# Kernel tuning notes

Measured on AMD Instinct MI355X. Metric: run time of the kernel, lower is better.

## Reference

```python
import jax, jax.numpy as jnp
import numpy as np

N_HEADS = 8
EPS = 1e-12  # F.normalize eps


def setup_inputs() -> dict:
    key = jax.random.key(0)
    ks = jax.random.split(key, 7)
    B, M, S, D = 2, 4, 2048, 512
    scale = 1.0 / np.sqrt(D)
    return {
        "x": jax.random.normal(ks[0], (B, M, S, D), dtype=jnp.float32),
        "Wq": jax.random.normal(ks[1], (D, D), dtype=jnp.float32) * scale,
        "bq": jax.random.normal(ks[2], (D,), dtype=jnp.float32) * 0.01,
        "Wkv": jax.random.normal(ks[3], (D, D), dtype=jnp.float32) * scale,
        "bkv": jax.random.normal(ks[4], (D,), dtype=jnp.float32) * 0.01,
        "Wo": jax.random.normal(ks[5], (D, D), dtype=jnp.float32) * scale,
        "bo": jax.random.normal(ks[6], (D,), dtype=jnp.float32) * 0.01,
    }


def _heads(t, H):
    # [B,M,S,D] -> [B,M,H,S,dk]
    B, Mo, S, D = t.shape
    return t.reshape(B, Mo, S, H, D // H).swapaxes(2, 3)


def reference(x, Wq, bq, Wkv, bkv, Wo, bo):
    B, Mo, S, D = x.shape
    H = N_HEADS
    # nn.Linear: y = x @ W^T + b
    Q = x @ Wq.T + bq
    KV = x @ Wkv.T + bkv  # K and V share this projection
    Qh = _heads(Q, H)
    Kh = _heads(KV, H)
    Vh = Kh
    # L2-normalize along head dim (cosine attention)
    Qn = Qh / jnp.maximum(jnp.linalg.norm(Qh, axis=-1, keepdims=True), EPS)
    Kn = Kh / jnp.maximum(jnp.linalg.norm(Kh, axis=-1, keepdims=True), EPS)
    scores = jnp.einsum("bmhqd,bmhkd->bmhqk", Qn, Kn)
    attn = jax.nn.softmax(scores, axis=-1)  # dropout=0 (eval)
    ctx = jnp.einsum("bmhqk,bmhkd->bmhqd", attn, Vh)
    ctx = ctx.swapaxes(2, 3).reshape(B, Mo, S, D)
    return ctx @ Wo.T + bo
```

## Files before the change

kernel.cpp:

```cpp
#include <hip/hip_runtime.h>

typedef __attribute__((ext_vector_type(8))) short bf16x8;
typedef __attribute__((ext_vector_type(8))) _Float16 f16x8;
typedef __attribute__((ext_vector_type(2))) _Float16 f16x2;
typedef __attribute__((ext_vector_type(4))) float f32x4;

__device__ __forceinline__ unsigned short f2bf(float f) {
  union { float f; unsigned int i; } v;
  v.f = f;
  unsigned int r = v.i + 0x7FFFu + ((v.i >> 16) & 1u);
  return (unsigned short)(r >> 16);
}

__device__ __forceinline__ f16x2 cvt_pk(float a, float b) {
  return __builtin_bit_cast(f16x2, __builtin_amdgcn_cvt_pkrtz(a, b));
}

__device__ __forceinline__ void gl_lds16(const unsigned short* g, unsigned short* l) {
  __builtin_amdgcn_global_load_lds(
      (const __attribute__((address_space(1))) unsigned int*)g,
      (__attribute__((address_space(3))) unsigned int*)l, 16, 0, 0);
}

__device__ __forceinline__ f16x2 exp_poly(f16x2 x) {
  const f16x2 a5 = {(_Float16)0.00868682f, (_Float16)0.00868682f};
  const f16x2 a4 = {(_Float16)0.04379392f, (_Float16)0.04379392f};
  const f16x2 a3 = {(_Float16)0.16648887f, (_Float16)0.16648887f};
  const f16x2 a2 = {(_Float16)0.49919676f, (_Float16)0.49919676f};
  const f16x2 a1 = {(_Float16)1.00002229f, (_Float16)1.00002229f};
  const f16x2 a0 = {(_Float16)1.00004478f, (_Float16)1.00004478f};
#if __has_builtin(__builtin_elementwise_fma)
  f16x2 r = a5;
  r = __builtin_elementwise_fma(r, x, a4);
  r = __builtin_elementwise_fma(r, x, a3);
  r = __builtin_elementwise_fma(r, x, a2);
  r = __builtin_elementwise_fma(r, x, a1);
  r = __builtin_elementwise_fma(r, x, a0);
#else
  f16x2 r = a5;
  r = r * x + a4;
  r = r * x + a3;
  r = r * x + a2;
  r = r * x + a1;
  r = r * x + a0;
#endif
  return r;
}

__global__ __launch_bounds__(256) void cvt_all(
    const float* __restrict__ x, const float* __restrict__ wq,
    const float* __restrict__ wkv, const float* __restrict__ wo,
    unsigned short* __restrict__ xf, unsigned short* __restrict__ wqf,
    unsigned short* __restrict__ wkvf, unsigned short* __restrict__ wof) {
  int b = blockIdx.x;
  const float* in;
  unsigned short* out;
  int i;
  if (b < 8192) { in = x; out = xf; i = b * 256 + threadIdx.x; }
  else if (b < 8448) { in = wq; out = wqf; i = (b - 8192) * 256 + threadIdx.x; }
  else if (b < 8704) { in = wkv; out = wkvf; i = (b - 8448) * 256 + threadIdx.x; }
  else { in = wo; out = wof; i = (b - 8704) * 256 + threadIdx.x; }
  float4 v = ((const float4*)in)[i];
  int f = i << 2;
  int row = f >> 9, c = f & 511;
  long off = ((((long)(row >> 7) * 8 + (c >> 6)) * 16 + ((row >> 4) & 7) * 2 +
               ((c >> 5) & 1)) * 64 + ((c >> 3) & 3) * 16 + (row & 15)) * 8 + (c & 7);
  ushort4 o;
  o.x = f2bf(v.x);
  o.y = f2bf(v.y);
  o.z = f2bf(v.z);
  o.w = f2bf(v.w);
  *(ushort4*)(out + off) = o;
}

__global__ __launch_bounds__(256) void gemm_qkv(
    const unsigned short* __restrict__ xf, const unsigned short* __restrict__ Wqf,
    const unsigned short* __restrict__ Wkvf, const float* __restrict__ bq,
    const float* __restrict__ bkv, unsigned short* __restrict__ Qn,
    unsigned short* __restrict__ Kf, unsigned short* __restrict__ Vf) {
  __shared__ __attribute__((aligned(16))) unsigned short lA[16 * 512];
  __shared__ __attribute__((aligned(16))) unsigned short lB[16 * 512];
  const int isKV = (int)(blockIdx.y >> 2);
  const unsigned short* Btf = isKV ? Wkvf : Wqf;
  const float* bias = isKV ? bkv : bq;
  const int tid = threadIdx.x;
  const int lane = tid & 63;
  const int quad = lane >> 4, m16 = lane & 15;
  const int w = tid >> 6;
  const int wm = w >> 1, wn = w & 1;
  const long mb = (long)blockIdx.x * 128;
  const int nt = (int)(blockIdx.y & 3);
  const long nb = (long)nt * 128;
  f32x4 acc[4][4];
#pragma unroll
  for (int i = 0; i < 4; i++)
#pragma unroll
    for (int j = 0; j < 4; j++) acc[i][j] = (f32x4){0.f, 0.f, 0.f, 0.f};

  for (int kb = 0; kb < 8; kb++) {
    __syncthreads();
    {
      const unsigned short* gA =
          xf + (((long)blockIdx.x * 8 + kb) * 16 + 4 * w) * 512 + lane * 8;
      gl_lds16(gA, &lA[(4 * w + 0) * 512]);
      gl_lds16(gA + 512, &lA[(4 * w + 1) * 512]);
      gl_lds16(gA + 1024, &lA[(4 * w + 2) * 512]);
      gl_lds16(gA + 1536, &lA[(4 * w + 3) * 512]);
      const unsigned short* gB =
          Btf + (((long)nt * 8 + kb) * 16 + 4 * w) * 512 + lane * 8;
      gl_lds16(gB, &lB[(4 * w + 0) * 512]);
      gl_lds16(gB + 512, &lB[(4 * w + 1) * 512]);
      gl_lds16(gB + 1024, &lB[(4 * w + 2) * 512]);
      gl_lds16(gB + 1536, &lB[(4 * w + 3) * 512]);
    }
    __syncthreads();
#pragma unroll
    for (int ks = 0; ks < 2; ks++) {
      bf16x8 af[4], bfr[4];
#pragma unroll
      for (int i = 0; i < 4; i++)
        af[i] = *(const bf16x8*)&lA[(((wm * 4 + i) << 1) | ks) * 512 + lane * 8];
#pragma unroll
      for (int j = 0; j < 4; j++)
        bfr[j] = *(const bf16x8*)&lB[(((wn * 4 + j) << 1) | ks) * 512 + lane * 8];
#pragma unroll
      for (int i = 0; i < 4; i++)
#pragma unroll
        for (int j = 0; j < 4; j++)
          acc[i][j] =
              __builtin_amdgcn_mfma_f32_16x16x32_bf16(af[i], bfr[j], acc[i][j], 0, 0, 0);
    }
  }
  const int h = (int)(nb >> 6) + wn;
#pragma unroll
  for (int i = 0; i < 4; i++) {
    long row0 = mb + wm * 64 + i * 16 + quad * 4;
    float bb[4], val[4][4], inv[4];
#pragma unroll
    for (int j = 0; j < 4; j++) {
      bb[j] = bias[nb + wn * 64 + j * 16 + m16];
#pragma unroll
      for (int r = 0; r < 4; r++) val[j][r] = acc[i][j][r] + bb[j];
    }
#pragma unroll
    for (int r = 0; r < 4; r++) {
      float s = val[0][r] * val[0][r] + val[1][r] * val[1][r] +
                val[2][r] * val[2][r] + val[3][r] * val[3][r];
      s += __shfl_xor(s, 1);
      s += __shfl_xor(s, 2);
      s += __shfl_xor(s, 4);
      s += __shfl_xor(s, 8);
      inv[r] = 1.0f / fmaxf(sqrtf(s), 1e-12f);
    }
    if (!isKV) {
#pragma unroll
      for (int r = 0; r < 4; r++)
#pragma unroll
        for (int j = 0; j < 4; j++) {
          long col = nb + wn * 64 + j * 16 + m16;
          Qn[(row0 + r) * 512 + col] = f2bf(val[j][r] * inv[r]);
        }
    } else {
      const int bm = (int)(row0 >> 11);
      const int g = bm * 8 + h;
      const int kt = (int)((row0 & 2047) >> 6);
      const long tb = ((long)g * 32 + kt) * 8;
#pragma unroll
      for (int j = 0; j < 4; j++) {
        long kb0 = (tb + i * 2 + (j >> 1)) * 512 +
                   (((((j & 1) << 1) | (m16 >> 3)) * 16 + quad * 4) * 8) + (m16 & 7);
#pragma unroll
        for (int r = 0; r < 4; r++) Kf[kb0 + r * 8] = f2bf(val[j][r] * inv[r]);
      }
#pragma unroll
      for (int j = 0; j < 4; j++) {
        long vo = (tb + j * 2 + (i >> 1)) * 512 +
                  ((((((i & 1) << 1) | (quad >> 1)) * 16 + m16)) * 8) + (quad & 1) * 4;
        f16x2 lo = cvt_pk(val[j][0], val[j][1]);
        f16x2 hi = cvt_pk(val[j][2], val[j][3]);
        uint2 pk = make_uint2(__builtin_bit_cast(unsigned int, lo),
                              __builtin_bit_cast(unsigned int, hi));
        *(uint2*)(Vf + vo) = pk;
      }
    }
  }
}

__global__ __launch_bounds__(256) void gemm_o(
    const unsigned short* __restrict__ Af, const unsigned short* __restrict__ Btf,
    const float* __restrict__ bias, float* __restrict__ Cout) {
  __shared__ __attribute__((aligned(16))) unsigned short lA[16 * 512];
  __shared__ __attribute__((aligned(16))) unsigned short lB[16 * 512];
  const int tid = threadIdx.x;
  const int lane = tid & 63;
  const int quad = lane >> 4, m16 = lane & 15;
  const int w = tid >> 6;
  const int wm = w >> 1, wn = w & 1;
  const long mb = (long)blockIdx.x * 128;
  const int nt = (int)blockIdx.y;
  const long nb = (long)nt * 128;
  f32x4 acc[4][4];
#pragma unroll
  for (int i = 0; i < 4; i++)
#pragma unroll
    for (int j = 0; j < 4; j++) acc[i][j] = (f32x4){0.f, 0.f, 0.f, 0.f};

  for (int kb = 0; kb < 8; kb++) {
    __syncthreads();
    {
      const unsigned short* gA =
          Af + (((long)blockIdx.x * 8 + kb) * 16 + 4 * w) * 512 + lane * 8;
      gl_lds16(gA, &lA[(4 * w + 0) * 512]);
      gl_lds16(gA + 512, &lA[(4 * w + 1) * 512]);
      gl_lds16(gA + 1024, &lA[(4 * w + 2) * 512]);
      gl_lds16(gA + 1536, &lA[(4 * w + 3) * 512]);
      const unsigned short* gB =
          Btf + (((long)nt * 8 + kb) * 16 + 4 * w) * 512 + lane * 8;
      gl_lds16(gB, &lB[(4 * w + 0) * 512]);
      gl_lds16(gB + 512, &lB[(4 * w + 1) * 512]);
      gl_lds16(gB + 1024, &lB[(4 * w + 2) * 512]);
      gl_lds16(gB + 1536, &lB[(4 * w + 3) * 512]);
    }
    __syncthreads();
#pragma unroll
    for (int ks = 0; ks < 2; ks++) {
      bf16x8 af[4], bfr[4];
#pragma unroll
      for (int i = 0; i < 4; i++)
        af[i] = *(const bf16x8*)&lA[(((wm * 4 + i) << 1) | ks) * 512 + lane * 8];
#pragma unroll
      for (int j = 0; j < 4; j++)
        bfr[j] = *(const bf16x8*)&lB[(((wn * 4 + j) << 1) | ks) * 512 + lane * 8];
#pragma unroll
      for (int i = 0; i < 4; i++)
#pragma unroll
        for (int j = 0; j < 4; j++)
          acc[i][j] =
              __builtin_amdgcn_mfma_f32_16x16x32_bf16(af[i], bfr[j], acc[i][j], 0, 0, 0);
    }
  }
#pragma unroll
  for (int i = 0; i < 4; i++) {
    long row0 = mb + wm * 64 + i * 16 + quad * 4;
#pragma unroll
    for (int j = 0; j < 4; j++) {
      long col = nb + wn * 64 + j * 16 + m16;
      float bb = bias[col];
#pragma unroll
      for (int r = 0; r < 4; r++) Cout[(row0 + r) * 512 + col] = acc[i][j][r] + bb;
    }
  }
}

__global__ __launch_bounds__(512, 4) void attn_cos(
    const unsigned short* __restrict__ Qn, const unsigned short* __restrict__ Kf,
    const unsigned short* __restrict__ Vf, unsigned short* __restrict__ ctxf) {
  __shared__ __attribute__((aligned(16))) unsigned short lK[2][8 * 512];
  __shared__ __attribute__((aligned(16))) unsigned short lVt[2][8 * 512];
  __shared__ __attribute__((aligned(16))) unsigned short lP[256 * 64];
  const int id = (int)blockIdx.x;
  const int g = ((id >> 6) << 3) | (id & 7);
  const int qt = (id >> 3) & 7;
  const int bm = g >> 3, h = g & 7;
  const int tid = threadIdx.x;
  const int lane = tid & 63;
  const int quad = lane >> 4, m16 = lane & 15;
  const int w = tid >> 6;
  const long qrow0 = (long)bm * 2048 + qt * 256 + w * 32;
  const int colbase = h * 64;
  const int swz = (m16 & 7) << 3;
  unsigned short* myP = lP + (w * 32) * 64;

  bf16x8 qf[2][2];
#pragma unroll
  for (int i = 0; i < 2; i++)
#pragma unroll
    for (int ks = 0; ks < 2; ks++)
      qf[i][ks] = *(const bf16x8*)(Qn + (qrow0 + i * 16 + m16) * 512 + colbase +
                                   ks * 32 + quad * 8);

  f32x4 cacc[2][4];
#pragma unroll
  for (int i = 0; i < 2; i++)
#pragma unroll
    for (int j = 0; j < 4; j++) cacc[i][j] = (f32x4){0.f, 0.f, 0.f, 0.f};
  f32x4 cacc_l[2];
  cacc_l[0] = (f32x4){0.f, 0.f, 0.f, 0.f};
  cacc_l[1] = (f32x4){0.f, 0.f, 0.f, 0.f};
  const f16x8 onesv = {(_Float16)1.0f, (_Float16)1.0f, (_Float16)1.0f, (_Float16)1.0f,
                       (_Float16)1.0f, (_Float16)1.0f, (_Float16)1.0f, (_Float16)1.0f};

  {
    const long tb0 = (long)g * 32 * 8;
    gl_lds16(Kf + (tb0 + w) * 512 + lane * 8, &lK[0][w * 512]);
    gl_lds16(Vf + (tb0 + w) * 512 + lane * 8, &lVt[0][w * 512]);
  }
  __syncthreads();

  int cur = 0;
  for (int kt = 0; kt < 32; ++kt) {
    {
      const int ktn = (kt + 1) & 31;
      const long tbn = ((long)g * 32 + ktn) * 8;
      gl_lds16(Kf + (tbn + w) * 512 + lane * 8, &lK[cur ^ 1][w * 512]);
      gl_lds16(Vf + (tbn + w) * 512 + lane * 8, &lVt[cur ^ 1][w * 512]);
    }

    f32x4 sacc[2][4];
#pragma unroll
    for (int i = 0; i < 2; i++)
#pragma unroll
      for (int j = 0; j < 4; j++) sacc[i][j] = (f32x4){0.f, 0.f, 0.f, 0.f};
#pragma unroll
    for (int ks = 0; ks < 2; ++ks) {
      bf16x8 kfr[4];
#pragma unroll
      for (int j = 0; j < 4; j++)
        kfr[j] = *(const bf16x8*)&lK[cur][((j << 1) | ks) * 512 + lane * 8];
#pragma unroll
      for (int j = 0; j < 4; j++)
#pragma unroll
        for (int i = 0; i < 2; i++)
          sacc[i][j] = __builtin_amdgcn_mfma_f32_16x16x32_bf16(kfr[j], qf[i][ks],
                                                               sacc[i][j], 0, 0, 0);
    }

#pragma unroll
    for (int i = 0; i < 2; i++)
#pragma unroll
      for (int j = 0; j < 4; j++) {
        f16x2 x01 = cvt_pk(sacc[i][j][0], sacc[i][j][1]);
        f16x2 x23 = cvt_pk(sacc[i][j][2], sacc[i][j][3]);
        f16x2 e01 = exp_poly(x01);
        f16x2 e23 = exp_poly(x23);
        uint2 pk2 = make_uint2(__builtin_bit_cast(unsigned int, e01),
                               __builtin_bit_cast(unsigned int, e23));
        *(uint2*)&myP[(i * 16 + m16) * 64 + ((j * 16 + quad * 4) ^ swz)] = pk2;
      }

#pragma unroll
    for (int ks = 0; ks < 2; ++ks) {
      f16x8 vfr[4];
#pragma unroll
      for (int j = 0; j < 4; j++)
        vfr[j] = *(const f16x8*)&lVt[cur][((j << 1) | ks) * 512 + lane * 8];
      f16x8 pfr[2];
#pragma unroll
      for (int i = 0; i < 2; i++)
        pfr[i] = *(const f16x8*)&myP[(i * 16 + m16) * 64 +
                                     ((ks * 32 + quad * 8) ^ swz)];
#pragma unroll
      for (int i = 0; i < 2; i++) {
#pragma unroll
        for (int j = 0; j < 4; j++)
          cacc[i][j] = __builtin_amdgcn_mfma_f32_16x16x32_f16(pfr[i], vfr[j],
                                                              cacc[i][j], 0, 0, 0);
        cacc_l[i] =
            __builtin_amdgcn_mfma_f32_16x16x32_f16(pfr[i], onesv, cacc_l[i], 0, 0, 0);
      }
    }

    __syncthreads();
    cur ^= 1;
  }

  float linv[2][4];
#pragma unroll
  for (int i = 0; i < 2; i++)
#pragma unroll
    for (int r = 0; r < 4; r++) linv[i][r] = 1.0f / cacc_l[i][r];
  const long cb0 = (((long)(bm * 16 + qt * 2 + (w >> 2)) * 8 + h) * 16);
#pragma unroll
  for (int i = 0; i < 2; i++)
#pragma unroll
    for (int j = 0; j < 4; j++) {
      long off = (cb0 + ((w & 3) * 2 + i) * 2 + (j >> 1)) * 512 +
                 (((((j & 1) << 1) | (m16 >> 3)) * 16 + quad * 4) * 8) + (m16 & 7);
#pragma unroll
      for (int r = 0; r < 4; r++)
        ctxf[off + r * 8] = f2bf(cacc[i][j][r] * linv[i][r]);
    }
}

extern "C" void kernel_launch(void* const* d_in, const int* in_sizes, int n_in,
                              void* d_out, int out_size, void* d_ws, size_t ws_size,
                              hipStream_t stream) {
  (void)in_sizes; (void)n_in; (void)out_size; (void)ws_size;
  const float* x = (const float*)d_in[0];
  const float* Wq = (const float*)d_in[1];
  const float* bq = (const float*)d_in[2];
  const float* Wkv = (const float*)d_in[3];
  const float* bkv = (const float*)d_in[4];
  const float* Wo = (const float*)d_in[5];
  const float* bo = (const float*)d_in[6];

  char* ws = (char*)d_ws;
  unsigned short* xf     = (unsigned short*)(ws);
  unsigned short* Wqf    = (unsigned short*)(ws + 16777216);
  unsigned short* Wkvf   = (unsigned short*)(ws + 17301504);
  unsigned short* Wof    = (unsigned short*)(ws + 17825792);
  unsigned short* Qn_bf  = (unsigned short*)(ws + 18350080);
  unsigned short* Kf     = (unsigned short*)(ws + 35127296);
  unsigned short* Vf     = (unsigned short*)(ws + 51904512);
  unsigned short* ctxf   = xf;

  cvt_all<<<8960, 256, 0, stream>>>(x, Wq, Wkv, Wo, xf, Wqf, Wkvf, Wof);

  gemm_qkv<<<dim3(128, 8), 256, 0, stream>>>(xf, Wqf, Wkvf, bq, bkv, Qn_bf, Kf, Vf);

  attn_cos<<<512, 512, 0, stream>>>(Qn_bf, Kf, Vf, ctxf);

  gemm_o<<<dim3(128, 4), 256, 0, stream>>>(ctxf, Wof, bo, (float*)d_out);
}
```

Measured before the change: 219.7 us.

## Switch attention to 32x32x16 MFMA and keep P in registers via permlane swap

Result: slower. 229.6 us (+4.5%).

```diff
diff --git a/kernel.cpp b/kernel.cpp
--- a/kernel.cpp
+++ b/kernel.cpp
@@ -4,6 +4,8 @@
 typedef __attribute__((ext_vector_type(8))) _Float16 f16x8;
 typedef __attribute__((ext_vector_type(2))) _Float16 f16x2;
 typedef __attribute__((ext_vector_type(4))) float f32x4;
+typedef __attribute__((ext_vector_type(16))) float f32x16;
+typedef __attribute__((ext_vector_type(2))) unsigned int u32x2;
 
 __device__ __forceinline__ unsigned short f2bf(float f) {
   union { float f; unsigned int i; } v;
@@ -14,6 +16,35 @@
 
 __device__ __forceinline__ f16x2 cvt_pk(float a, float b) {
   return __builtin_bit_cast(f16x2, __builtin_amdgcn_cvt_pkrtz(a, b));
+}
+
+__device__ __forceinline__ unsigned as_u32(f16x2 x) {
+  return __builtin_bit_cast(unsigned int, x);
+}
+__device__ __forceinline__ f16x2 as_f16x2(unsigned x) {
+  return __builtin_bit_cast(f16x2, x);
+}
+
+#if __has_builtin(__builtin_amdgcn_permlane32_swap)
+__device__ __forceinline__ u32x2 plswap(unsigned a, unsigned b) {
+  return __builtin_amdgcn_permlane32_swap(a, b, false, false);
+}
+#else
+__device__ __forceinline__ u32x2 plswap(unsigned a, unsigned b) {
+  unsigned pa = (unsigned)__shfl_xor((int)a, 32);
+  unsigned pb = (unsigned)__shfl_xor((int)b, 32);
+  int hi = (int)(threadIdx.x & 32);
+  u32x2 r;
+  r.x = hi ? pb : a;
+  r.y = hi ? b : pa;
+  return r;
+}
+#endif
+
+__device__ __forceinline__ f16x8 pack4(f16x2 a, f16x2 b, f16x2 c, f16x2 d) {
+  union { f16x2 h[4]; f16x8 v; } u;
+  u.h[0] = a; u.h[1] = b; u.h[2] = c; u.h[3] = d;
+  return u.v;
 }
 
 __device__ __forceinline__ void gl_lds16(const unsigned short* g, unsigned short* l) {
@@ -45,6 +76,15 @@
   r = r * x + a0;
 #endif
   return r;
+}
+
+__device__ __forceinline__ float dot2acc(f16x2 a, float acc) {
+#if __has_builtin(__builtin_amdgcn_fdot2)
+  const f16x2 one2 = {(_Float16)1.0f, (_Float16)1.0f};
+  return __builtin_amdgcn_fdot2(a, one2, acc, false);
+#else
+  return acc + (float)a.x + (float)a.y;
+#endif
 }
 
 __global__ __launch_bounds__(256) void cvt_all(
@@ -161,25 +201,25 @@
           Qn[(row0 + r) * 512 + col] = f2bf(val[j][r] * inv[r]);
         }
     } else {
-      const int bm = (int)(row0 >> 11);
-      const int g = bm * 8 + h;
+      const int bm2 = (int)(row0 >> 11);
+      const int gq = bm2 * 8 + h;
       const int kt = (int)((row0 & 2047) >> 6);
-      const long tb = ((long)g * 32 + kt) * 8;
+      const long tb = ((long)gq * 32 + kt) * 8;
 #pragma unroll
       for (int j = 0; j < 4; j++) {
-        long kb0 = (tb + i * 2 + (j >> 1)) * 512 +
-                   (((((j & 1) << 1) | (m16 >> 3)) * 16 + quad * 4) * 8) + (m16 & 7);
+        long kb0 = (tb + (i >> 1) * 4 + j) * 512 +
+                   ((((i & 1) * 16 + quad * 4) | ((m16 >> 3) << 5)) * 8) + (m16 & 7);
 #pragma unroll
         for (int r = 0; r < 4; r++) Kf[kb0 + r * 8] = f2bf(val[j][r] * inv[r]);
       }
 #pragma unroll
       for (int j = 0; j < 4; j++) {
-        long vo = (tb + j * 2 + (i >> 1)) * 512 +
-                  ((((((i & 1) << 1) | (quad >> 1)) * 16 + m16)) * 8) + (quad & 1) * 4;
+        long vo = (tb + (j >> 1) * 4 + i) * 512 +
+                  ((((j & 1) * 16 + m16) | ((quad >> 1) << 5)) * 8) + (quad & 1) * 4;
         f16x2 lo = cvt_pk(val[j][0], val[j][1]);
-        f16x2 hi = cvt_pk(val[j][2], val[j][3]);
+        f16x2 hi2 = cvt_pk(val[j][2], val[j][3]);
         uint2 pk = make_uint2(__builtin_bit_cast(unsigned int, lo),
-                              __builtin_bit_cast(unsigned int, hi));
+                              __builtin_bit_cast(unsigned int, hi2));
         *(uint2*)(Vf + vo) = pk;
       }
     }
@@ -257,38 +297,26 @@
     const unsigned short* __restrict__ Vf, unsigned short* __restrict__ ctxf) {
   __shared__ __attribute__((aligned(16))) unsigned short lK[2][8 * 512];
   __shared__ __attribute__((aligned(16))) unsigned short lVt[2][8 * 512];
-  __shared__ __attribute__((aligned(16))) unsigned short lP[256 * 64];
   const int id = (int)blockIdx.x;
   const int g = ((id >> 6) << 3) | (id & 7);
   const int qt = (id >> 3) & 7;
   const int bm = g >> 3, h = g & 7;
   const int tid = threadIdx.x;
   const int lane = tid & 63;
-  const int quad = lane >> 4, m16 = lane & 15;
+  const int l31 = lane & 31, hi = lane >> 5;
   const int w = tid >> 6;
   const long qrow0 = (long)bm * 2048 + qt * 256 + w * 32;
   const int colbase = h * 64;
-  const int swz = (m16 & 7) << 3;
-  unsigned short* myP = lP + (w * 32) * 64;
-
-  bf16x8 qf[2][2];
-#pragma unroll
-  for (int i = 0; i < 2; i++)
-#pragma unroll
-    for (int ks = 0; ks < 2; ks++)
-      qf[i][ks] = *(const bf16x8*)(Qn + (qrow0 + i * 16 + m16) * 512 + colbase +
-                                   ks * 32 + quad * 8);
-
-  f32x4 cacc[2][4];
-#pragma unroll
-  for (int i = 0; i < 2; i++)
-#pragma unroll
-    for (int j = 0; j < 4; j++) cacc[i][j] = (f32x4){0.f, 0.f, 0.f, 0.f};
-  f32x4 cacc_l[2];
-  cacc_l[0] = (f32x4){0.f, 0.f, 0.f, 0.f};
-  cacc_l[1] = (f32x4){0.f, 0.f, 0.f, 0.f};
-  const f16x8 onesv = {(_Float16)1.0f, (_Float16)1.0f, (_Float16)1.0f, (_Float16)1.0f,
-                       (_Float16)1.0f, (_Float16)1.0f, (_Float16)1.0f, (_Float16)1.0f};
+
+  bf16x8 qf[4];
+#pragma unroll
+  for (int dd = 0; dd < 4; dd++)
+    qf[dd] = *(const bf16x8*)(Qn + (qrow0 + l31) * 512 + colbase + dd * 16 + hi * 8);
+
+  f32x16 cacc[2];
+#pragma unroll
+  for (int e = 0; e < 16; e++) { cacc[0][e] = 0.f; cacc[1][e] = 0.f; }
+  float lacc = 0.f;
 
   {
     const long tb0 = (long)g * 32 * 8;
@@ -306,80 +334,68 @@
       gl_lds16(Vf + (tbn + w) * 512 + lane * 8, &lVt[cur ^ 1][w * 512]);
     }
 
-    f32x4 sacc[2][4];
-#pragma unroll
-    for (int i = 0; i < 2; i++)
-#pragma unroll
-      for (int j = 0; j < 4; j++) sacc[i][j] = (f32x4){0.f, 0.f, 0.f, 0.f};
-#pragma unroll
-    for (int ks = 0; ks < 2; ++ks) {
-      bf16x8 kfr[4];
-#pragma unroll
-      for (int j = 0; j < 4; j++)
-        kfr[j] = *(const bf16x8*)&lK[cur][((j << 1) | ks) * 512 + lane * 8];
-#pragma unroll
-      for (int j = 0; j < 4; j++)
-#pragma unroll
-        for (int i = 0; i < 2; i++)
-          sacc[i][j] = __builtin_amdgcn_mfma_f32_16x16x32_bf16(kfr[j], qf[i][ks],
-                                                               sacc[i][j], 0, 0, 0);
-    }
-
-#pragma unroll
-    for (int i = 0; i < 2; i++)
-#pragma unroll
-      for (int j = 0; j < 4; j++) {
-        f16x2 x01 = cvt_pk(sacc[i][j][0], sacc[i][j][1]);
-        f16x2 x23 = cvt_pk(sacc[i][j][2], sacc[i][j][3]);
-        f16x2 e01 = exp_poly(x01);
-        f16x2 e23 = exp_poly(x23);
-        uint2 pk2 = make_uint2(__builtin_bit_cast(unsigned int, e01),
-                               __builtin_bit_cast(unsigned int, e23));
-        *(uint2*)&myP[(i * 16 + m16) * 64 + ((j * 16 + quad * 4) ^ swz)] = pk2;
+    f32x16 sacc[2];
+#pragma unroll
+    for (int e = 0; e < 16; e++) { sacc[0][e] = 0.f; sacc[1][e] = 0.f; }
+#pragma unroll
+    for (int dd = 0; dd < 4; dd++) {
+      bf16x8 k0 = *(const bf16x8*)&lK[cur][(0 * 4 + dd) * 512 + lane * 8];
+      bf16x8 k1 = *(const bf16x8*)&lK[cur][(1 * 4 + dd) * 512 + lane * 8];
+      sacc[0] = __builtin_amdgcn_mfma_f32_32x32x16_bf16(k0, qf[dd], sacc[0], 0, 0, 0);
+      sacc[1] = __builtin_amdgcn_mfma_f32_32x32x16_bf16(k1, qf[dd], sacc[1], 0, 0, 0);
+    }
+
+    f16x2 pe[2][8];
+#pragma unroll
+    for (int kk = 0; kk < 2; kk++)
+#pragma unroll
+      for (int t = 0; t < 8; t++) {
+        f16x2 x = cvt_pk(sacc[kk][2 * t], sacc[kk][2 * t + 1]);
+        pe[kk][t] = exp_poly(x);
+        lacc = dot2acc(pe[kk][t], lacc);
       }
 
 #pragma unroll
-    for (int ks = 0; ks < 2; ++ks) {
-      f16x8 vfr[4];
-#pragma unroll
-      for (int j = 0; j < 4; j++)
-        vfr[j] = *(const f16x8*)&lVt[cur][((j << 1) | ks) * 512 + lane * 8];
-      f16x8 pfr[2];
-#pragma unroll
-      for (int i = 0; i < 2; i++)
-        pfr[i] = *(const f16x8*)&myP[(i * 16 + m16) * 64 +
-                                     ((ks * 32 + quad * 8) ^ swz)];
-#pragma unroll
-      for (int i = 0; i < 2; i++) {
-#pragma unroll
-        for (int j = 0; j < 4; j++)
-          cacc[i][j] = __builtin_amdgcn_mfma_f32_16x16x32_f16(pfr[i], vfr[j],
-                                                              cacc[i][j], 0, 0, 0);
-        cacc_l[i] =
-            __builtin_amdgcn_mfma_f32_16x16x32_f16(pfr[i], onesv, cacc_l[i], 0, 0, 0);
+    for (int kk = 0; kk < 2; kk++)
+#pragma unroll
+      for (int s = 0; s < 2; s++) {
+        u32x2 r0 = plswap(as_u32(pe[kk][4 * s + 0]), as_u32(pe[kk][4 * s + 2]));
+        u32x2 r1 = plswap(as_u32(pe[kk][4 * s + 1]), as_u32(pe[kk][4 * s + 3]));
+        f16x8 pa = pack4(as_f16x2(r0.x), as_f16x2(r1.x), as_f16x2(r0.y), as_f16x2(r1.y));
+        const int ksub = kk * 2 + s;
+        f16x8 v0 = *(const f16x8*)&lVt[cur][(0 * 4 + ksub) * 512 + lane * 8];
+        f16x8 v1 = *(const f16x8*)&lVt[cur][(1 * 4 + ksub) * 512 + lane * 8];
+        cacc[0] = __builtin_amdgcn_mfma_f32_32x32x16_f16(pa, v0, cacc[0], 0, 0, 0);
+        cacc[1] = __builtin_amdgcn_mfma_f32_32x32x16_f16(pa, v1, cacc[1], 0, 0, 0);
       }
-    }
 
     __syncthreads();
     cur ^= 1;
   }
 
-  float linv[2][4];
-#pragma unroll
-  for (int i = 0; i < 2; i++)
-#pragma unroll
-    for (int r = 0; r < 4; r++) linv[i][r] = 1.0f / cacc_l[i][r];
-  const long cb0 = (((long)(bm * 16 + qt * 2 + (w >> 2)) * 8 + h) * 16);
-#pragma unroll
-  for (int i = 0; i < 2; i++)
-#pragma unroll
-    for (int j = 0; j < 4; j++) {
-      long off = (cb0 + ((w & 3) * 2 + i) * 2 + (j >> 1)) * 512 +
-                 (((((j & 1) << 1) | (m16 >> 3)) * 16 + quad * 4) * 8) + (m16 & 7);
-#pragma unroll
-      for (int r = 0; r < 4; r++)
-        ctxf[off + r * 8] = f2bf(cacc[i][j][r] * linv[i][r]);
-    }
+  lacc += __shfl_xor(lacc, 32);
+  float linv[16];
+#pragma unroll
+  for (int r = 0; r < 16; r++) {
+    int qr = (r & 3) + 8 * (r >> 2) + 4 * hi;
+    linv[r] = 1.0f / __shfl(lacc, qr);
+  }
+
+#pragma unroll
+  for (int dt = 0; dt < 2; dt++) {
+    const int c = colbase + dt * 32 + l31;
+    const long ckb = (long)(c >> 6);
+    const int cbit = (c >> 5) & 1;
+    const int lane16 = ((c >> 3) & 3) * 16;
+    const int e = c & 7;
+#pragma unroll
+    for (int r = 0; r < 16; r++) {
+      long row = qrow0 + (r & 3) + 8 * (r >> 2) + 4 * hi;
+      long off = ((((row >> 7) * 8 + ckb) * 16 + ((row >> 4) & 7) * 2 + cbit) * 64 +
+                  lane16 + (row & 15)) * 8 + e;
+      ctxf[off] = f2bf(cacc[dt][r] * linv[r]);
+    }
+  }
 }
 
 extern "C" void kernel_launch(void* const* d_in, const int* in_sizes, int n_in,
```
